# Kernel tuning notes

Hardware: AMD Instinct MI355X
Metric: run time of the kernel (lower is better)

## Reference

```python
import jax, jax.numpy as jnp
import numpy as np

N_CONFIGS = 8
N_NODES = 100000
N_EDGES = 400000
N_GRAPHS = 10
FEAT_DIM = 97          # 1 op-code column + 96 float features
OP_EMB = 32
MAX_OP_CODE = 128
D_IN = OP_EMB + FEAT_DIM - 1   # 128
HIDDEN = 64


def setup_inputs() -> dict:
    key = jax.random.key(0)
    ks = jax.random.split(key, 10)
    features = jax.random.normal(ks[0], (N_CONFIGS, N_NODES, FEAT_DIM), dtype=jnp.float32)
    op_codes = jax.random.randint(ks[1], (N_CONFIGS, N_NODES), 0, MAX_OP_CODE)
    features = features.at[..., 0].set(op_codes.astype(jnp.float32))
    edge_index = jax.random.randint(ks[2], (2, N_EDGES), 0, N_NODES, dtype=jnp.int32)
    lengths = jnp.full((N_GRAPHS,), N_NODES // N_GRAPHS, dtype=jnp.int32)
    s = 1.0 / np.sqrt(D_IN)
    emb_table = jax.random.normal(ks[3], (MAX_OP_CODE, OP_EMB), dtype=jnp.float32)
    W1 = jax.random.normal(ks[4], (D_IN, HIDDEN), dtype=jnp.float32) * s
    b1 = jnp.zeros((HIDDEN,), dtype=jnp.float32)
    W2 = jax.random.normal(ks[5], (HIDDEN, HIDDEN), dtype=jnp.float32) / np.sqrt(HIDDEN)
    b2 = jnp.zeros((HIDDEN,), dtype=jnp.float32)
    Wp = jax.random.normal(ks[6], (HIDDEN, 1), dtype=jnp.float32) / np.sqrt(HIDDEN)
    bp = jnp.zeros((1,), dtype=jnp.float32)
    return {"features": features, "edge_index": edge_index, "lengths": lengths,
            "emb_table": emb_table, "W1": W1, "b1": b1, "W2": W2, "b2": b2,
            "Wp": Wp, "bp": bp}


def reference(features, edge_index, lengths, emb_table, W1, b1, W2, b2, Wp, bp):
    C, N, _ = features.shape
    src, dst = edge_index[0], edge_index[1]
    # row-normalized sparse adjacency values (mean aggregation), no grad needed
    deg = jax.ops.segment_sum(jnp.ones_like(src, dtype=jnp.float32), src, num_segments=N)
    vals = 1.0 / jnp.clip(deg, 1.0)[src]              # [E]

    # embedding input layer: embed op code (col 0), concat remaining features
    op = features[..., 0].astype(jnp.int32)           # [C, N]
    x = jnp.concatenate([emb_table[op], features[..., 1:]], axis=-1)  # [C, N, D_IN]

    def spmm(h):  # (A_norm @ h) per config: out[src] += vals * h[dst]
        msg = h[:, dst, :] * vals[None, :, None]      # [C, E, D]
        return jnp.zeros((C, N, h.shape[-1]), h.dtype).at[:, src, :].add(msg)

    # message passing layers
    x = jax.nn.relu(spmm(x) @ W1 + b1)                # [C, N, HIDDEN]
    x = jax.nn.relu(spmm(x) @ W2 + b2)                # [C, N, HIDDEN]

    # projection -> per-node runtime, abs (exp=False)
    r = jnp.abs(x @ Wp + bp)                          # [C, N, 1]

    # per-graph scatter-sum pooling over nodes
    G = lengths.shape[0]
    index = jnp.repeat(jnp.arange(G), lengths, total_repeat_length=N)  # [N]
    pooled = jnp.zeros((C, G, 1), r.dtype).at[:, index, :].add(r)      # [C, G, 1]
    return jnp.squeeze(jnp.transpose(pooled, (1, 0, 2)))               # [G, C]
```

## Files before the change

kernel.cpp:

```cpp
#include <hip/hip_runtime.h>

#define NCFG 8
#define NN 100000
#define NE 400000
#define NG 10
#define FEAT 97
#define SCAN_BLOCKS 25

typedef __attribute__((ext_vector_type(8))) short bf16x8;
typedef __attribute__((ext_vector_type(4))) float f32x4;

__device__ inline short f2bf(float x){
  unsigned u = __float_as_uint(x);
  unsigned r = u + 0x7FFFu + ((u >> 16) & 1u);
  return (short)(r >> 16);
}
__device__ inline float bf2f(short h){
  return __uint_as_float(((unsigned)(unsigned short)h) << 16);
}

__global__ void k_hist(const int* __restrict__ src, int* __restrict__ deg, int e_count){
  int e = blockIdx.x*blockDim.x + threadIdx.x;
  if(e < e_count) atomicAdd(&deg[src[e]], 1);
}

__global__ __launch_bounds__(1024) void k_scanA(const int* __restrict__ deg,
    int* __restrict__ partial, int n){
  __shared__ int ws[16];
  int tid = threadIdx.x;
  int i0 = blockIdx.x*4096 + tid*4;
  int s = 0;
  #pragma unroll
  for(int i=0;i<4;i++) if(i0+i < n) s += deg[i0+i];
  #pragma unroll
  for(int off=1; off<64; off<<=1) s += __shfl_xor(s, off, 64);
  if((tid & 63) == 0) ws[tid >> 6] = s;
  __syncthreads();
  if(tid < 16){
    int v = ws[tid];
    #pragma unroll
    for(int off=1; off<16; off<<=1) v += __shfl_xor(v, off, 16);
    if(tid == 0) partial[blockIdx.x] = v;
  }
}

__global__ void k_scanB(int* __restrict__ partial, int* __restrict__ rowptr, int nb, int n){
  int tid = threadIdx.x;
  int v = (tid < nb) ? partial[tid] : 0;
  int x = v;
  #pragma unroll
  for(int off=1; off<64; off<<=1){
    int t = __shfl_up(x, off, 64);
    if(tid >= off) x += t;
  }
  if(tid < nb) partial[tid] = x - v;
  if(tid == nb-1) rowptr[n] = x;
}

__global__ __launch_bounds__(1024) void k_scanC(int* __restrict__ deg_cur,
    const int* __restrict__ partial, int* __restrict__ rowptr,
    float* __restrict__ inv_deg, int n){
  __shared__ int wsum[16];
  int tid = threadIdx.x, lane = tid & 63, w = tid >> 6;
  int i0 = blockIdx.x*4096 + tid*4;
  int v0 = (i0+0 < n) ? deg_cur[i0+0] : 0;
  int v1 = (i0+1 < n) ? deg_cur[i0+1] : 0;
  int v2 = (i0+2 < n) ? deg_cur[i0+2] : 0;
  int v3 = (i0+3 < n) ? deg_cur[i0+3] : 0;
  int s = v0+v1+v2+v3;
  int x = s;
  #pragma unroll
  for(int off=1; off<64; off<<=1){
    int t = __shfl_up(x, off, 64);
    if(lane >= off) x += t;
  }
  if(lane == 63) wsum[w] = x;
  __syncthreads();
  if(w == 0){
    int y = (lane < 16) ? wsum[lane] : 0;
    #pragma unroll
    for(int off=1; off<16; off<<=1){
      int t = __shfl_up(y, off, 64);
      if(lane >= off) y += t;
    }
    if(lane < 16) wsum[lane] = y;
  }
  __syncthreads();
  int waveoff = (w > 0) ? wsum[w-1] : 0;
  int run = partial[blockIdx.x] + waveoff + (x - s);
  if(i0+0 < n){ rowptr[i0+0]=run; deg_cur[i0+0]=run; inv_deg[i0+0]=1.0f/(float)max(v0,1); run+=v0; }
  if(i0+1 < n){ rowptr[i0+1]=run; deg_cur[i0+1]=run; inv_deg[i0+1]=1.0f/(float)max(v1,1); run+=v1; }
  if(i0+2 < n){ rowptr[i0+2]=run; deg_cur[i0+2]=run; inv_deg[i0+2]=1.0f/(float)max(v2,1); run+=v2; }
  if(i0+3 < n){ rowptr[i0+3]=run; deg_cur[i0+3]=run; inv_deg[i0+3]=1.0f/(float)max(v3,1); run+=v3; }
}

__global__ void k_fill(const int* __restrict__ src, const int* __restrict__ dst,
                       int* __restrict__ cursor, int* __restrict__ col, int e_count){
  int e = blockIdx.x*blockDim.x + threadIdx.x;
  if(e < e_count){
    int pos = atomicAdd(&cursor[src[e]], 1);
    col[pos] = dst[e];
  }
}

__global__ void k_embW1(const float* __restrict__ emb, const float* __restrict__ W1,
                        float* __restrict__ embW1){
  int o = blockIdx.x, j = threadIdx.x;
  float s = 0.f;
  #pragma unroll
  for(int k=0;k<32;k++) s += emb[o*32+k] * W1[k*64+j];
  embW1[o*64+j] = s;
}

__global__ void k_offsets(const int* __restrict__ lengths, int* __restrict__ off){
  if(threadIdx.x == 0){
    int s = 0;
    for(int g=0; g<NG; g++){ off[g] = s; s += lengths[g]; }
    off[NG] = s;
  }
}

__global__ __launch_bounds__(256) void k_prepB(const float* __restrict__ W1, const float* __restrict__ W2,
    short* __restrict__ bW1hi, short* __restrict__ bW1lo,
    short* __restrict__ bW2hi, short* __restrict__ bW2lo){
  int e = blockIdx.x*256 + threadIdx.x;
  if(e < 3*4*64*8){
    int i=e&7, l=(e>>3)&63, t=(e>>9)&3, kc=e>>11;
    int k=kc*32+((l>>4)<<3)+i, c=t*16+(l&15);
    float wv = W1[(32+k)*64+c];
    short h=f2bf(wv); bW1hi[e]=h; bW1lo[e]=f2bf(wv-bf2f(h));
  }
  if(e < 2*4*64*8){
    int i=e&7, l=(e>>3)&63, t=(e>>9)&3, kc=e>>11;
    int k=kc*32+((l>>4)<<3)+i, c=t*16+(l&15);
    float wv = W2[k*64+c];
    short h=f2bf(wv); bW2hi[e]=h; bW2lo[e]=f2bf(wv-bf2f(h));
  }
}

__global__ __launch_bounds__(256) void k_gemm1(const float* __restrict__ feat,
    const float* __restrict__ embW1,
    const short* __restrict__ bW1hi, const short* __restrict__ bW1lo,
    unsigned short* __restrict__ z_all){
  __shared__ float lds_f[64*FEAT];
  int tid = threadIdx.x;
  int nb = blockIdx.x * 64;
  int cfg = blockIdx.y;
  const float* f = feat + (size_t)cfg*NN*FEAT;
  const float* gsrc = f + (size_t)nb*FEAT;
  int nvalid = (min(64, NN-nb))*FEAT;

  for(int idx = tid; idx < 1552; idx += 256){
    int base = idx*4;
    float4 v;
    if(base + 3 < nvalid) v = *(const float4*)(gsrc + base);
    else {
      v.x = (base+0 < nvalid) ? gsrc[base+0] : 0.f;
      v.y = (base+1 < nvalid) ? gsrc[base+1] : 0.f;
      v.z = (base+2 < nvalid) ? gsrc[base+2] : 0.f;
      v.w = (base+3 < nvalid) ? gsrc[base+3] : 0.f;
    }
    *(float4*)&lds_f[base] = v;
  }
  __syncthreads();

  int w = tid >> 6, l = tid & 63;
  int lrow = w*16 + (l & 15);
  int g8 = (l >> 4) << 3;

  f32x4 acc[4] = {{0,0,0,0},{0,0,0,0},{0,0,0,0},{0,0,0,0}};
  #pragma unroll
  for(int kc = 0; kc < 3; kc++){
    const float* ap = &lds_f[lrow*FEAT + 1 + g8 + kc*32];
    bf16x8 ahi, alo;
    #pragma unroll
    for(int i=0;i<8;i++){
      float a = ap[i];
      short h = f2bf(a);
      ahi[i] = h;
      alo[i] = f2bf(a - bf2f(h));
    }
    #pragma unroll
    for(int t=0;t<4;t++){
      const bf16x8 bh = *(const bf16x8*)&bW1hi[((kc*4 + t)*64 + l)*8];
      const bf16x8 bl = *(const bf16x8*)&bW1lo[((kc*4 + t)*64 + l)*8];
      acc[t] = __builtin_amdgcn_mfma_f32_16x16x32_bf16(ahi, bh, acc[t], 0,0,0);
      acc[t] = __builtin_amdgcn_mfma_f32_16x16x32_bf16(alo, bh, acc[t], 0,0,0);
      acc[t] = __builtin_amdgcn_mfma_f32_16x16x32_bf16(ahi, bl, acc[t], 0,0,0);
    }
  }
  int r0 = w*16 + ((l>>4)<<2);
  int cb = l & 15;
  #pragma unroll
  for(int j=0;j<4;j++){
    int node = nb + r0 + j;
    if(node < NN){
      int op = (int)lds_f[(r0+j)*FEAT];
      #pragma unroll
      for(int t=0;t<4;t++){
        int c = t*16 + cb;
        z_all[((size_t)node*NCFG + cfg)*64 + c] = (unsigned short)f2bf(acc[t][j] + embW1[op*64 + c]);
      }
    }
  }
}

__global__ __launch_bounds__(256) void k_gather1(const int* __restrict__ rowptr,
    const int* __restrict__ col, const float* __restrict__ inv_deg,
    const unsigned short* __restrict__ z_all, const float* __restrict__ b1,
    unsigned short* __restrict__ h_all){
  int tid = threadIdx.x, lane = tid & 63;
  int n = (blockIdx.x << 2) + (tid >> 6);
  if(n >= NN) return;
  int sub = lane & 7;
  const unsigned short* zl = z_all + lane*8;
  int kb = __builtin_amdgcn_readfirstlane(rowptr[n]);
  int ke = __builtin_amdgcn_readfirstlane(rowptr[n+1]);
  float acc[8] = {0,0,0,0,0,0,0,0};
  for(int k = kb; k < ke; k++){
    int d = __builtin_amdgcn_readfirstlane(col[k]);
    const bf16x8 v = *(const bf16x8*)(zl + (size_t)d*512);
    #pragma unroll
    for(int i=0;i<8;i++) acc[i] += bf2f(v[i]);
  }
  float inv = inv_deg[n];
  const float4 bA = *(const float4*)(b1 + sub*8);
  const float4 bB = *(const float4*)(b1 + sub*8 + 4);
  float bv[8] = {bA.x,bA.y,bA.z,bA.w,bB.x,bB.y,bB.z,bB.w};
  bf16x8 o;
  #pragma unroll
  for(int i=0;i<8;i++) o[i] = f2bf(fmaxf(fmaf(acc[i], inv, bv[i]), 0.f));
  *(bf16x8*)(h_all + (size_t)n*512 + lane*8) = o;
}

__global__ __launch_bounds__(256) void k_gather2W(const int* __restrict__ rowptr,
    const int* __restrict__ col, const float* __restrict__ inv_deg,
    const unsigned short* __restrict__ h_all,
    const short* __restrict__ bW2hi, const short* __restrict__ bW2lo,
    const float* __restrict__ b2, const float* __restrict__ Wp,
    const float* __restrict__ bp, float* __restrict__ r_all){
  __shared__ unsigned short V[128][68];
  int tid = threadIdx.x, lane = tid & 63, w = tid >> 6;
  int nb = blockIdx.x * 16;
  int cfg = lane >> 3, sub = lane & 7;
  const unsigned short* hl = h_all + lane*8;

  for(int i = 0; i < 4; i++){
    int nl = w*4 + i;
    int n = nb + nl;
    int kb = __builtin_amdgcn_readfirstlane(rowptr[n]);
    int ke = __builtin_amdgcn_readfirstlane(rowptr[n+1]);
    float acc[8] = {0,0,0,0,0,0,0,0};
    for(int k = kb; k < ke; k++){
      int d = __builtin_amdgcn_readfirstlane(col[k]);
      const bf16x8 v = *(const bf16x8*)(hl + (size_t)d*512);
      #pragma unroll
      for(int j=0;j<8;j++) acc[j] += bf2f(v[j]);
    }
    float inv = inv_deg[n];
    bf16x8 o;
    #pragma unroll
    for(int j=0;j<8;j++) o[j] = f2bf(acc[j] * inv);
    *(bf16x8*)&V[nl*8 + cfg][sub*8] = o;
  }
  __syncthreads();

  float bp0 = bp[0];
  int cb = lane & 15;
  int koff = (lane >> 4) << 3;
  #pragma unroll
  for(int at = 0; at < 2; at++){
    int tile = w*2 + at;
    int trow = tile*16 + cb;
    f32x4 acc[4] = {{0,0,0,0},{0,0,0,0},{0,0,0,0},{0,0,0,0}};
    #pragma unroll
    for(int kc = 0; kc < 2; kc++){
      const bf16x8 a = *(const bf16x8*)&V[trow][kc*32 + koff];
      #pragma unroll
      for(int t=0;t<4;t++){
        const bf16x8 bh = *(const bf16x8*)&bW2hi[((kc*4+t)*64 + lane)*8];
        const bf16x8 bl = *(const bf16x8*)&bW2lo[((kc*4+t)*64 + lane)*8];
        acc[t] = __builtin_amdgcn_mfma_f32_16x16x32_bf16(a, bh, acc[t], 0,0,0);
        acc[t] = __builtin_amdgcn_mfma_f32_16x16x32_bf16(a, bl, acc[t], 0,0,0);
      }
    }
    float part[4];
    #pragma unroll
    for(int j=0;j<4;j++){
      float p = 0.f;
      #pragma unroll
      for(int t=0;t<4;t++){
        int c = t*16 + cb;
        p += fmaxf(acc[t][j] + b2[c], 0.f) * Wp[c];
      }
      part[j] = p;
    }
    #pragma unroll
    for(int off=1; off<16; off<<=1){
      #pragma unroll
      for(int j=0;j<4;j++) part[j] += __shfl_xor(part[j], off, 64);
    }
    if(cb == 0){
      #pragma unroll
      for(int j=0;j<4;j++){
        int row = tile*16 + ((lane>>4)<<2) + j;
        int node = nb + (row >> 3);
        int cfgo = row & 7;
        r_all[(size_t)cfgo*NN + node] = fabsf(part[j] + bp0);
      }
    }
  }
}

__global__ __launch_bounds__(256) void k_pool(const float* __restrict__ r_all,
    const int* __restrict__ off, float* __restrict__ out){
  __shared__ float red[256];
  int b = blockIdx.x;
  int g = b >> 3, c = b & 7;
  int lo = off[g], hi = off[g+1];
  float s = 0.f;
  for(int i = lo + (int)threadIdx.x; i < hi; i += 256) s += r_all[(size_t)c*NN + i];
  red[threadIdx.x] = s;
  __syncthreads();
  for(int w=128; w>0; w>>=1){
    if((int)threadIdx.x < w) red[threadIdx.x] += red[threadIdx.x + w];
    __syncthreads();
  }
  if(threadIdx.x == 0) out[b] = red[0];
}

extern "C" void kernel_launch(void* const* d_in, const int* in_sizes, int n_in,
                              void* d_out, int out_size, void* d_ws, size_t ws_size,
                              hipStream_t stream){
  (void)in_sizes; (void)n_in; (void)out_size; (void)ws_size;
  const float* feat = (const float*)d_in[0];
  const int*   eidx = (const int*)d_in[1];
  const int*   lens = (const int*)d_in[2];
  const float* emb  = (const float*)d_in[3];
  const float* W1   = (const float*)d_in[4];
  const float* b1   = (const float*)d_in[5];
  const float* W2   = (const float*)d_in[6];
  const float* b2   = (const float*)d_in[7];
  const float* Wp   = (const float*)d_in[8];
  const float* bp   = (const float*)d_in[9];
  float* out = (float*)d_out;
  const int* src = eidx;
  const int* dst = eidx + NE;

  char* ws = (char*)d_ws;
  size_t o = 0;
  auto alloc = [&](size_t bytes)->char*{ char* p = ws + o; o = (o + bytes + 255) & ~(size_t)255; return p; };
  int*   rowptr  = (int*)  alloc((NN+1)*4);
  int*   cursor  = (int*)  alloc((size_t)NN*4);
  int*   colx    = (int*)  alloc((size_t)NE*4);
  float* invd    = (float*)alloc((size_t)NN*4);
  int*   goff    = (int*)  alloc((NG+1)*4);
  int*   spart   = (int*)  alloc(SCAN_BLOCKS*4);
  float* eW1     = (float*)alloc(128*64*4);
  short* bW1hi   = (short*)alloc(3*4*64*8*2);
  short* bW1lo   = (short*)alloc(3*4*64*8*2);
  short* bW2hi   = (short*)alloc(2*4*64*8*2);
  short* bW2lo   = (short*)alloc(2*4*64*8*2);
  float* r_all   = (float*)alloc((size_t)NCFG*NN*4);
  unsigned short* z_all = (unsigned short*)alloc((size_t)NN*NCFG*64*2);
  unsigned short* h_all = (unsigned short*)alloc((size_t)NN*NCFG*64*2);

  hipMemsetAsync(cursor, 0, (size_t)NN*4, stream);
  k_hist   <<<(NE+255)/256, 256, 0, stream>>>(src, cursor, NE);
  k_scanA  <<<SCAN_BLOCKS, 1024, 0, stream>>>(cursor, spart, NN);
  k_scanB  <<<1, 64, 0, stream>>>(spart, rowptr, SCAN_BLOCKS, NN);
  k_scanC  <<<SCAN_BLOCKS, 1024, 0, stream>>>(cursor, spart, rowptr, invd, NN);
  k_fill   <<<(NE+255)/256, 256, 0, stream>>>(src, dst, cursor, colx, NE);
  k_embW1  <<<128, 64, 0, stream>>>(emb, W1, eW1);
  k_prepB  <<<24, 256, 0, stream>>>(W1, W2, bW1hi, bW1lo, bW2hi, bW2lo);
  k_offsets<<<1, 64, 0, stream>>>(lens, goff);

  dim3 ggemm((NN+63)/64, NCFG);
  k_gemm1  <<<ggemm, 256, 0, stream>>>(feat, eW1, bW1hi, bW1lo, z_all);
  k_gather1<<<(NN+3)/4, 256, 0, stream>>>(rowptr, colx, invd, z_all, b1, h_all);
  k_gather2W<<<NN/16, 256, 0, stream>>>(rowptr, colx, invd, h_all, bW2hi, bW2lo, b2, Wp, bp, r_all);
  k_pool   <<<NCFG*NG, 256, 0, stream>>>(r_all, goff, out);
}
```

Before: 367.9 us.

## Unroll gather loops 4x, cut GEMM1 precision passes, vectorize z stores

Both neighbor-gather loops are unrolled by four with separate accumulators, so four independent row loads are in flight per iteration instead of one serial load chain. GEMM1 drops the low-part feature term: features go to bf16 once and only the two MFMAs on the hi/lo weight split remain, with operands swapped so each lane owns a node row and can write packed ushort4 z outputs. A fast path without bounds checks handles full feature tiles. The price is reduced precision in layer 1, since features are no longer split into hi/lo parts, and higher register pressure in the gathers.

```diff
diff --git a/kernel.cpp b/kernel.cpp
--- a/kernel.cpp
+++ b/kernel.cpp
@@ -146,61 +146,59 @@
   int tid = threadIdx.x;
   int nb = blockIdx.x * 64;
   int cfg = blockIdx.y;
-  const float* f = feat + (size_t)cfg*NN*FEAT;
-  const float* gsrc = f + (size_t)nb*FEAT;
-  int nvalid = (min(64, NN-nb))*FEAT;
-
-  for(int idx = tid; idx < 1552; idx += 256){
-    int base = idx*4;
-    float4 v;
-    if(base + 3 < nvalid) v = *(const float4*)(gsrc + base);
-    else {
+  const float* gsrc = feat + ((size_t)cfg*NN + nb)*FEAT;
+
+  if(nb + 64 <= NN){
+    for(int idx = tid; idx < 1552; idx += 256)
+      *(float4*)&lds_f[idx*4] = *(const float4*)(gsrc + idx*4);
+  } else {
+    int nvalid = (NN - nb)*FEAT;
+    for(int idx = tid; idx < 1552; idx += 256){
+      int base = idx*4;
+      float4 v;
       v.x = (base+0 < nvalid) ? gsrc[base+0] : 0.f;
       v.y = (base+1 < nvalid) ? gsrc[base+1] : 0.f;
       v.z = (base+2 < nvalid) ? gsrc[base+2] : 0.f;
       v.w = (base+3 < nvalid) ? gsrc[base+3] : 0.f;
-    }
-    *(float4*)&lds_f[base] = v;
+      *(float4*)&lds_f[base] = v;
+    }
   }
   __syncthreads();
 
   int w = tid >> 6, l = tid & 63;
-  int lrow = w*16 + (l & 15);
+  int node_loc = w*16 + (l & 15);
   int g8 = (l >> 4) << 3;
 
   f32x4 acc[4] = {{0,0,0,0},{0,0,0,0},{0,0,0,0},{0,0,0,0}};
   #pragma unroll
   for(int kc = 0; kc < 3; kc++){
-    const float* ap = &lds_f[lrow*FEAT + 1 + g8 + kc*32];
-    bf16x8 ahi, alo;
-    #pragma unroll
-    for(int i=0;i<8;i++){
-      float a = ap[i];
-      short h = f2bf(a);
-      ahi[i] = h;
-      alo[i] = f2bf(a - bf2f(h));
-    }
+    const float* ap = &lds_f[node_loc*FEAT + 1 + g8 + kc*32];
+    bf16x8 bfeat;
+    #pragma unroll
+    for(int i=0;i<8;i++) bfeat[i] = f2bf(ap[i]);
     #pragma unroll
     for(int t=0;t<4;t++){
-      const bf16x8 bh = *(const bf16x8*)&bW1hi[((kc*4 + t)*64 + l)*8];
-      const bf16x8 bl = *(const bf16x8*)&bW1lo[((kc*4 + t)*64 + l)*8];
-      acc[t] = __builtin_amdgcn_mfma_f32_16x16x32_bf16(ahi, bh, acc[t], 0,0,0);
-      acc[t] = __builtin_amdgcn_mfma_f32_16x16x32_bf16(alo, bh, acc[t], 0,0,0);
-      acc[t] = __builtin_amdgcn_mfma_f32_16x16x32_bf16(ahi, bl, acc[t], 0,0,0);
-    }
-  }
-  int r0 = w*16 + ((l>>4)<<2);
-  int cb = l & 15;
-  #pragma unroll
-  for(int j=0;j<4;j++){
-    int node = nb + r0 + j;
-    if(node < NN){
-      int op = (int)lds_f[(r0+j)*FEAT];
-      #pragma unroll
-      for(int t=0;t<4;t++){
-        int c = t*16 + cb;
-        z_all[((size_t)node*NCFG + cfg)*64 + c] = (unsigned short)f2bf(acc[t][j] + embW1[op*64 + c]);
-      }
+      const bf16x8 ah = *(const bf16x8*)&bW1hi[((kc*4 + t)*64 + l)*8];
+      const bf16x8 al = *(const bf16x8*)&bW1lo[((kc*4 + t)*64 + l)*8];
+      acc[t] = __builtin_amdgcn_mfma_f32_16x16x32_bf16(ah, bfeat, acc[t], 0,0,0);
+      acc[t] = __builtin_amdgcn_mfma_f32_16x16x32_bf16(al, bfeat, acc[t], 0,0,0);
+    }
+  }
+  int node = nb + node_loc;
+  int g = l >> 4;
+  if(node < NN){
+    int op = (int)lds_f[node_loc*FEAT];
+    unsigned short* zrow = z_all + ((size_t)node*NCFG + cfg)*64;
+    #pragma unroll
+    for(int t=0;t<4;t++){
+      int f0 = t*16 + g*4;
+      const float4 e = *(const float4*)&embW1[op*64 + f0];
+      ushort4 pk;
+      pk.x = (unsigned short)f2bf(acc[t][0] + e.x);
+      pk.y = (unsigned short)f2bf(acc[t][1] + e.y);
+      pk.z = (unsigned short)f2bf(acc[t][2] + e.z);
+      pk.w = (unsigned short)f2bf(acc[t][3] + e.w);
+      *(ushort4*)(zrow + f0) = pk;
     }
   }
 }
@@ -214,14 +212,27 @@
   if(n >= NN) return;
   int sub = lane & 7;
   const unsigned short* zl = z_all + lane*8;
-  int kb = __builtin_amdgcn_readfirstlane(rowptr[n]);
-  int ke = __builtin_amdgcn_readfirstlane(rowptr[n+1]);
-  float acc[8] = {0,0,0,0,0,0,0,0};
-  for(int k = kb; k < ke; k++){
-    int d = __builtin_amdgcn_readfirstlane(col[k]);
+  int kb = rowptr[n], ke = rowptr[n+1];
+  float a0[8]={0,0,0,0,0,0,0,0}, a1[8]={0,0,0,0,0,0,0,0};
+  float a2[8]={0,0,0,0,0,0,0,0}, a3[8]={0,0,0,0,0,0,0,0};
+  int k = kb;
+  for(; k+4 <= ke; k += 4){
+    int d0=col[k], d1=col[k+1], d2=col[k+2], d3=col[k+3];
+    const bf16x8 v0 = *(const bf16x8*)(zl + (size_t)d0*512);
+    const bf16x8 v1 = *(const bf16x8*)(zl + (size_t)d1*512);
+    const bf16x8 v2 = *(const bf16x8*)(zl + (size_t)d2*512);
+    const bf16x8 v3 = *(const bf16x8*)(zl + (size_t)d3*512);
+    #pragma unroll
+    for(int i=0;i<8;i++){
+      a0[i] += bf2f(v0[i]); a1[i] += bf2f(v1[i]);
+      a2[i] += bf2f(v2[i]); a3[i] += bf2f(v3[i]);
+    }
+  }
+  for(; k < ke; k++){
+    int d = col[k];
     const bf16x8 v = *(const bf16x8*)(zl + (size_t)d*512);
     #pragma unroll
-    for(int i=0;i<8;i++) acc[i] += bf2f(v[i]);
+    for(int i=0;i<8;i++) a0[i] += bf2f(v[i]);
   }
   float inv = inv_deg[n];
   const float4 bA = *(const float4*)(b1 + sub*8);
@@ -229,7 +240,10 @@
   float bv[8] = {bA.x,bA.y,bA.z,bA.w,bB.x,bB.y,bB.z,bB.w};
   bf16x8 o;
   #pragma unroll
-  for(int i=0;i<8;i++) o[i] = f2bf(fmaxf(fmaf(acc[i], inv, bv[i]), 0.f));
+  for(int i=0;i<8;i++){
+    float acc = (a0[i]+a1[i]) + (a2[i]+a3[i]);
+    o[i] = f2bf(fmaxf(fmaf(acc, inv, bv[i]), 0.f));
+  }
   *(bf16x8*)(h_all + (size_t)n*512 + lane*8) = o;
 }
 
@@ -248,19 +262,35 @@
   for(int i = 0; i < 4; i++){
     int nl = w*4 + i;
     int n = nb + nl;
-    int kb = __builtin_amdgcn_readfirstlane(rowptr[n]);
-    int ke = __builtin_amdgcn_readfirstlane(rowptr[n+1]);
-    float acc[8] = {0,0,0,0,0,0,0,0};
-    for(int k = kb; k < ke; k++){
-      int d = __builtin_amdgcn_readfirstlane(col[k]);
+    int kb = rowptr[n], ke = rowptr[n+1];
+    float a0[8]={0,0,0,0,0,0,0,0}, a1[8]={0,0,0,0,0,0,0,0};
+    float a2[8]={0,0,0,0,0,0,0,0}, a3[8]={0,0,0,0,0,0,0,0};
+    int k = kb;
+    for(; k+4 <= ke; k += 4){
+      int d0=col[k], d1=col[k+1], d2=col[k+2], d3=col[k+3];
+      const bf16x8 v0 = *(const bf16x8*)(hl + (size_t)d0*512);
+      const bf16x8 v1 = *(const bf16x8*)(hl + (size_t)d1*512);
+      const bf16x8 v2 = *(const bf16x8*)(hl + (size_t)d2*512);
+      const bf16x8 v3 = *(const bf16x8*)(hl + (size_t)d3*512);
+      #pragma unroll
+      for(int j=0;j<8;j++){
+        a0[j] += bf2f(v0[j]); a1[j] += bf2f(v1[j]);
+        a2[j] += bf2f(v2[j]); a3[j] += bf2f(v3[j]);
+      }
+    }
+    for(; k < ke; k++){
+      int d = col[k];
       const bf16x8 v = *(const bf16x8*)(hl + (size_t)d*512);
       #pragma unroll
-      for(int j=0;j<8;j++) acc[j] += bf2f(v[j]);
+      for(int j=0;j<8;j++) a0[j] += bf2f(v[j]);
     }
     float inv = inv_deg[n];
     bf16x8 o;
     #pragma unroll
-    for(int j=0;j<8;j++) o[j] = f2bf(acc[j] * inv);
+    for(int j=0;j<8;j++){
+      float acc = (a0[j]+a1[j]) + (a2[j]+a3[j]);
+      o[j] = f2bf(acc * inv);
+    }
     *(bf16x8*)&V[nl*8 + cfg][sub*8] = o;
   }
   __syncthreads();
```

New measurement: 367.0 us. About the same (-0.2%).
